# Kernel tuning notes

Hardware: AMD Instinct MI355X
Metric: run time of the kernel (lower is better)

The kernel has to match this reference:

```python
import jax, jax.numpy as jnp
import numpy as np

N, E, B, D, V = 200000, 3200000, 512, 32, 101
STEPS_MP, STEPS_S2S = 6, 6


def setup_inputs() -> dict:
    key = jax.random.key(0)
    ks = jax.random.split(key, 24)
    p = lambda k, s: jax.random.normal(k, s, jnp.float32) * 0.1
    inp = {}
    inp["node_type"] = jax.random.randint(ks[0], (N,), 0, V)
    inp["src"] = jax.random.randint(ks[1], (E,), 0, N)
    inp["dst"] = jax.random.randint(ks[2], (E,), 0, N)
    inp["graph_ids"] = jnp.sort(jax.random.randint(ks[3], (N,), 0, B))
    inp["emb"] = p(ks[4], (V, D)).at[0].set(0.0)  # padding_idx=0
    inp["W0"] = p(ks[5], (D, D)); inp["b0"] = p(ks[6], (D,))
    inp["Wm"] = p(ks[7], (D, D))
    inp["Wih_g"] = p(ks[8], (3 * D, D)); inp["Whh_g"] = p(ks[9], (3 * D, D))
    inp["bih_g"] = p(ks[10], (3 * D,)); inp["bhh_g"] = p(ks[11], (3 * D,))
    inp["Wih0"] = p(ks[12], (4 * D, 2 * D)); inp["Whh0"] = p(ks[13], (4 * D, D))
    inp["bih0"] = p(ks[14], (4 * D,)); inp["bhh0"] = p(ks[15], (4 * D,))
    inp["Wih12"] = p(ks[16], (2, 4 * D, D)); inp["Whh12"] = p(ks[17], (2, 4 * D, D))
    inp["bih12"] = p(ks[18], (2, 4 * D)); inp["bhh12"] = p(ks[19], (2, 4 * D))
    inp["Wr1"] = p(ks[20], (D, 2 * D)); inp["br1"] = p(ks[21], (D,))
    inp["Wr2"] = p(ks[22], (D, D)); inp["br2"] = p(ks[23], (D,))
    return inp


def _gru(x, h, Wih, Whh, bih, bhh):
    gi = x @ Wih.T + bih
    gh = h @ Whh.T + bhh
    r = jax.nn.sigmoid(gi[:, :D] + gh[:, :D])
    z = jax.nn.sigmoid(gi[:, D:2 * D] + gh[:, D:2 * D])
    n = jnp.tanh(gi[:, 2 * D:] + r * gh[:, 2 * D:])
    return (1.0 - z) * n + z * h


def _lstm(x, h, c, Wih, Whh, bih, bhh):
    g = x @ Wih.T + bih + h @ Whh.T + bhh
    i, f, gg, o = jnp.split(g, 4, axis=-1)  # torch gate order i,f,g,o
    c2 = jax.nn.sigmoid(f) * c + jax.nn.sigmoid(i) * jnp.tanh(gg)
    return jax.nn.sigmoid(o) * jnp.tanh(c2), c2


def _seg_softmax(e, ids, nseg):
    m = jax.ops.segment_max(e, ids, num_segments=nseg)
    ex = jnp.exp(e - m[ids])
    s = jax.ops.segment_sum(ex, ids, num_segments=nseg)
    return ex / s[ids]


def _forward(node_type, src, dst, graph_ids, emb, W0, b0, Wm,
             Wih_g, Whh_g, bih_g, bhh_g,
             Wih0, Whh0, bih0, bhh0, Wih12, Whh12, bih12, bhh12,
             Wr1, br1, Wr2, br2):
    # embedding lookup; dropout is identity at inference
    nfeat = emb[node_type]                         # [N, D]
    out = jax.nn.relu(nfeat @ W0.T + b0)           # lin0
    h = out                                        # GRU hidden init
    for _ in range(STEPS_MP):
        # NNConv-style sum aggregation over in-edges (e_feat is None -> edge-independent Wm)
        agg = jax.ops.segment_sum(out[src], dst, num_segments=N)   # [N, D]
        m = jax.nn.relu(agg @ Wm.T)
        h = _gru(m, h, Wih_g, Whh_g, bih_g, bhh_g)
        out = h
    # ---- Set2Set pooling (3-layer LSTM, 6 steps) ----
    lp = [(Wih0, Whh0, bih0, bhh0),
          (Wih12[0], Whh12[0], bih12[0], bhh12[0]),
          (Wih12[1], Whh12[1], bih12[1], bhh12[1])]
    hs = [jnp.zeros((B, D), out.dtype) for _ in range(3)]
    cs = [jnp.zeros((B, D), out.dtype) for _ in range(3)]
    q_star = jnp.zeros((B, 2 * D), out.dtype)
    for _ in range(STEPS_S2S):
        x = q_star
        for l, (Wih, Whh, bih, bhh) in enumerate(lp):
            hs[l], cs[l] = _lstm(x, hs[l], cs[l], Wih, Whh, bih, bhh)
            x = hs[l]
        q = x                                        # [B, D]
        e = jnp.sum(out * q[graph_ids], axis=-1)     # [N] attention logits
        alpha = _seg_softmax(e, graph_ids, B)
        r = jax.ops.segment_sum(alpha[:, None] * out, graph_ids, num_segments=B)
        q_star = jnp.concatenate([q, r], axis=-1)    # [B, 2D]
    # readout MLP (norm=False)
    return jax.nn.relu(q_star @ Wr1.T + br1) @ Wr2.T + br2


def reference(node_type, src, dst, graph_ids, emb, W0, b0, Wm,
              Wih_g, Whh_g, bih_g, bhh_g,
              Wih0, Whh0, bih0, bhh0, Wih12, Whh12, bih12, bhh12,
              Wr1, br1, Wr2, br2):
    return _forward(node_type, src, dst, graph_ids, emb, W0, b0, Wm,
                    Wih_g, Whh_g, bih_g, bhh_g,
                    Wih0, Whh0, bih0, bhh0, Wih12, Whh12, bih12, bhh12,
                    Wr1, br1, Wr2, br2)
```

## Files before the change

kernel.cpp:

```cpp
#include <hip/hip_runtime.h>
#include <hip/hip_bf16.h>
#include <hip/hip_fp16.h>

#define DD 32
constexpr int N_ = 200000;
constexpr int E_ = 3200000;
constexpr int B_ = 512;
constexpr int IDXCAP = 768;

typedef _Float16 f16x4 __attribute__((ext_vector_type(4)));
typedef float f32x4 __attribute__((ext_vector_type(4)));

constexpr int OFF_EMB=0, OFF_B0=3232, OFF_BIHG=3264, OFF_BHHG=3360, OFF_BIH0=3456,
  OFF_BHH0=3584, OFF_BIH12=3712, OFF_BHH12=3968, OFF_BR1=4224, OFF_BR2=4256,
  OFF_W0T=4288, OFF_WMT=5312, OFF_WIHGT=6336, OFF_WHHGT=9408,
  OFF_WIH0T=12480, OFF_WHH0T=20672, OFF_WIH1T=24768, OFF_WHH1T=28864,
  OFF_WIH2T=32960, OFF_WHH2T=37056, OFF_WR1T=41152, OFF_WR2T=43200;
constexpr long FLOAT_END=44288L;
constexpr size_t F16_BYTE = (size_t)FLOAT_END*4;
constexpr size_t H0_BYTE  = F16_BYTE + 12288;
constexpr size_t H1_BYTE  = H0_BYTE + (size_t)N_*DD*2;
constexpr size_t INT_BASE = H1_BYTE + (size_t)N_*DD*2;
constexpr int I_DEG=0, I_NOFF=200512, I_CURSOR=400512, I_GOFF=600512,
  I_BSUM=601088, I_BOFF=601344, I_CSR=601600;
constexpr int I_FLAG=3801600;

__device__ __forceinline__ float bf2f(unsigned short u){ return __uint_as_float(((unsigned)u)<<16); }
__device__ __forceinline__ float sigm(float x){ return 1.0f/(1.0f+__expf(-x)); }
__device__ __forceinline__ float tanhfast(float x){ return 1.0f - 2.0f/(__expf(2.0f*x)+1.0f); }

__device__ __forceinline__ void gbatch(const int* __restrict__ ip, int i, int rem,
                                       const __half* __restrict__ rowbase, int q,
                                       float& a0, float& a1, float& a2, float& a3){
  #pragma unroll
  for(int s=0;s<8;s++){
    int e  = 4*s + q;
    int ec = e < rem ? e : rem-1;
    int idx = ip[i + ec];
    uint2 v = *(const uint2*)(rowbase + (size_t)idx*DD);
    if(e >= rem){ v.x = 0u; v.y = 0u; }
    float2 f0 = __half22float2(*(__half2*)&v.x);
    float2 f1 = __half22float2(*(__half2*)&v.y);
    a0 += f0.x; a1 += f0.y; a2 += f1.x; a3 += f1.y;
  }
}

__global__ void k_detect(const unsigned int* __restrict__ emb_raw, int* __restrict__ flag){
  if(threadIdx.x==0){
    unsigned v=0;
    for(int i=16;i<32;i++) v |= emb_raw[i];
    flag[0] = v ? 1 : 0;
  }
}

struct PrepArgs { const void* s[22]; int off[22]; int sz[22]; int trR[22]; int soff[22]; int pk[22]; };

__global__ void k_prep(PrepArgs a, float* __restrict__ W, const int* __restrict__ flag){
  int bf = flag[0];
  int seg = blockIdx.y;
  int i = blockIdx.x*256 + threadIdx.x;
  if(i >= a.sz[seg]) return;
  int R = a.trR[seg];
  int P = a.pk[seg];
  int sidx;
  if(P){
    int c = i/(4*P); int rem = i%(4*P); int col = rem>>2; int s = rem&3;
    sidx = col*DD + 4*c + s;
  } else if(R){ int C = a.sz[seg]/R; sidx = (i%R)*C + (i/R); } else sidx = i;
  sidx += a.soff[seg];
  float v = bf ? bf2f(((const unsigned short*)a.s[seg])[sidx])
               : ((const float*)a.s[seg])[sidx];
  W[a.off[seg]+i] = v;
}

__global__ void k_prep16(const float* __restrict__ Wall, __half* __restrict__ F){
  int id = blockIdx.x*256 + threadIdx.x;
  if(id >= 6144) return;
  int e  = id & 3;
  int l  = (id >> 2) & 63;
  int kh = (id >> 8) & 1;
  int tmp = id >> 9;
  int jt  = tmp % 6;
  int reg = tmp / 6;
  int j = 16*jt + (l & 15);
  int k = 16*kh + 4*(l >> 4) + e;
  int srcoff = (reg==0 ? OFF_WIHGT : OFF_WHHGT) + j*DD + k;
  F[id] = __float2half(Wall[srcoff]);
}

__global__ void k_lin0(const int* __restrict__ nt, const float* __restrict__ Wall,
                       __half* __restrict__ hmir){
  int n = blockIdx.x*blockDim.x + threadIdx.x;
  if(n >= N_) return;
  const float* er  = Wall + OFF_EMB + nt[n]*DD;
  const float* W0T = Wall + OFF_W0T;
  const float* b0  = Wall + OFF_B0;
  float m[DD];
  #pragma unroll
  for(int j=0;j<DD;j++) m[j]=b0[j];
  #pragma unroll 4
  for(int k=0;k<DD;k++){
    float xk = er[k];
    #pragma unroll
    for(int j=0;j<DD;j++) m[j] = __fmaf_rn(W0T[k*DD+j], xk, m[j]);
  }
  __half* hrow = hmir + (size_t)n*DD;
  #pragma unroll
  for(int j=0;j<DD;j++) hrow[j]=__float2half(fmaxf(m[j],0.f));
}

__global__ void k_deg(const int* __restrict__ dst, int* __restrict__ deg,
                      int* __restrict__ key){
  int e = blockIdx.x*blockDim.x + threadIdx.x;
  if(e < E_){
    int d = dst[e];
    int old = atomicAdd(&deg[d], 1);
    key[e] = d | (old << 18);
  }
}
__global__ void __launch_bounds__(1024) k_scanA(const int* __restrict__ deg,
                       int* __restrict__ incl, int* __restrict__ bsum){
  __shared__ int sh[1024];
  int g = blockIdx.x*1024 + threadIdx.x;
  int v = (g < N_) ? deg[g] : 0;
  sh[threadIdx.x]=v; __syncthreads();
  for(int o=1;o<1024;o<<=1){
    int a = (threadIdx.x>=o) ? sh[threadIdx.x-o] : 0;
    __syncthreads();
    sh[threadIdx.x]+=a;
    __syncthreads();
  }
  if(g < N_) incl[g]=sh[threadIdx.x];
  if(threadIdx.x==1023) bsum[blockIdx.x]=sh[1023];
}
__global__ void k_scanB(const int* __restrict__ bsum, int* __restrict__ boff){
  __shared__ int sh[256];
  int t=threadIdx.x;
  int v=(t<196)?bsum[t]:0;
  sh[t]=v; __syncthreads();
  for(int o=1;o<256;o<<=1){
    int a=(t>=o)?sh[t-o]:0; __syncthreads(); sh[t]+=a; __syncthreads();
  }
  if(t<196) boff[t]=sh[t]-v;
}
__global__ void __launch_bounds__(1024) k_scanC(const int* __restrict__ deg,
                       const int* __restrict__ boff, int* __restrict__ noff,
                       int* __restrict__ incl_cursor){
  int g = blockIdx.x*1024 + threadIdx.x;
  if(g >= N_) return;
  int ex = incl_cursor[g] - deg[g] + boff[g>>10];
  noff[g]=ex; incl_cursor[g]=ex;
}
__global__ void k_goff(const int* __restrict__ gid, int* __restrict__ goff){
  int g = blockIdx.x*256 + threadIdx.x;
  if(g > B_) return;
  int lo=0, hi=N_;
  while(lo<hi){ int mid=(lo+hi)>>1; if(gid[mid]<g) lo=mid+1; else hi=mid; }
  goff[g]=lo;
}
__global__ void k_scatter(const int* __restrict__ src, const int* __restrict__ key,
                          const int* __restrict__ noff, int* __restrict__ csr){
  int e = blockIdx.x*256 + threadIdx.x;
  int k = key[e];
  int d = k & 0x3FFFF;
  int p = noff[d] + (k >> 18);
  csr[p] = src[e];
}

__global__ void __launch_bounds__(256) k_step(const float* __restrict__ Wall,
                       const __half* __restrict__ F16, const int* __restrict__ noff,
                       const int* __restrict__ deg, const int* __restrict__ csr,
                       const __half* __restrict__ curh, __half* __restrict__ nxth){
  __shared__ __align__(16) float  lds_acc[4][4][DD];
  __shared__ __align__(16) __half lds_m[4][16][40];
  __shared__ int lds_idx[4][IDXCAP];
  __shared__ int lds_nd[4][32];
  const int t = threadIdx.x;
  const int w = t >> 6, l = t & 63;
  const int d = l & 31, half = l >> 5;
  const int q  = d >> 3;
  const int r8 = d & 7;
  const int n0 = blockIdx.x*64 + w*16;
  const float4* WmP = (const float4*)(Wall + OFF_WMT);
  const __half* rowbase = curh + 4*r8;
  if(l < 16){
    lds_nd[w][l]    = noff[n0+l];
    lds_nd[w][16+l] = deg[n0+l];
  }
  int s_begin = lds_nd[w][0];
  int total   = lds_nd[w][15] + lds_nd[w][31] - s_begin;
  int tc = total < IDXCAP ? total : IDXCAP;
  for(int i=l; i<tc; i+=64) lds_idx[w][i] = csr[s_begin+i];
  if(total <= IDXCAP){
    for(int pp=0;pp<4;pp++){
      int iA = 4*pp + half, iB = iA + 2;
      int sA = lds_nd[w][iA] - s_begin, lA = lds_nd[w][16+iA];
      int sB = lds_nd[w][iB] - s_begin, lB = lds_nd[w][16+iB];
      const int* ipA = &lds_idx[w][sA];
      const int* ipB = &lds_idx[w][sB];
      float aA0=0.f,aA1=0.f,aA2=0.f,aA3=0.f;
      float aB0=0.f,aB1=0.f,aB2=0.f,aB3=0.f;
      int ml = lA > lB ? lA : lB;
      for(int i=0; i<ml; i+=32){
        int rA = lA - i, rB = lB - i;
        if(rA > 0) gbatch(ipA, i, rA, rowbase, q, aA0,aA1,aA2,aA3);
        if(rB > 0) gbatch(ipB, i, rB, rowbase, q, aB0,aB1,aB2,aB3);
      }
      #pragma unroll
      for(int off=8; off<=16; off<<=1){
        aA0 += __shfl_xor(aA0, off, 32); aA1 += __shfl_xor(aA1, off, 32);
        aA2 += __shfl_xor(aA2, off, 32); aA3 += __shfl_xor(aA3, off, 32);
        aB0 += __shfl_xor(aB0, off, 32); aB1 += __shfl_xor(aB1, off, 32);
        aB2 += __shfl_xor(aB2, off, 32); aB3 += __shfl_xor(aB3, off, 32);
      }
      int lsrc = d >> 2;
      float vA0=__shfl(aA0,lsrc,32), vA1=__shfl(aA1,lsrc,32);
      float vA2=__shfl(aA2,lsrc,32), vA3=__shfl(aA3,lsrc,32);
      float vB0=__shfl(aB0,lsrc,32), vB1=__shfl(aB1,lsrc,32);
      float vB2=__shfl(aB2,lsrc,32), vB3=__shfl(aB3,lsrc,32);
      float accA = (d&1) ? ((d&2)? vA3 : vA1) : ((d&2)? vA2 : vA0);
      float accB = (d&1) ? ((d&2)? vB3 : vB1) : ((d&2)? vB2 : vB0);
      lds_acc[w][half][d]   = accA;
      lds_acc[w][2+half][d] = accB;
      const float4* acA = (const float4*)(&lds_acc[w][half][0]);
      const float4* acB = (const float4*)(&lds_acc[w][2+half][0]);
      float mA = 0.f, mB = 0.f;
      #pragma unroll
      for(int c=0;c<8;c++){
        float4 wv = WmP[c*32 + d];
        float4 avA = acA[c];
        float4 avB = acB[c];
        mA = __fmaf_rn(wv.x, avA.x, mA); mB = __fmaf_rn(wv.x, avB.x, mB);
        mA = __fmaf_rn(wv.y, avA.y, mA); mB = __fmaf_rn(wv.y, avB.y, mB);
        mA = __fmaf_rn(wv.z, avA.z, mA); mB = __fmaf_rn(wv.z, avB.z, mB);
        mA = __fmaf_rn(wv.w, avA.w, mA); mB = __fmaf_rn(wv.w, avB.w, mB);
      }
      lds_m[w][iA][d] = __float2half(fmaxf(mA, 0.f));
      lds_m[w][iB][d] = __float2half(fmaxf(mB, 0.f));
    }
  } else {
    for(int p=0;p<8;p++){
      int ni = 2*p + half;
      int s0 = lds_nd[w][ni];
      int len = lds_nd[w][16+ni];
      float a0=0.f, a1=0.f, a2=0.f, a3=0.f;
      for(int i=0; i<len; i+=32){
        int rem = len - i;
        gbatch(csr + s0, i, rem, rowbase, q, a0,a1,a2,a3);
      }
      #pragma unroll
      for(int off=8; off<=16; off<<=1){
        a0 += __shfl_xor(a0, off, 32);
        a1 += __shfl_xor(a1, off, 32);
        a2 += __shfl_xor(a2, off, 32);
        a3 += __shfl_xor(a3, off, 32);
      }
      float v0 = __shfl(a0, d>>2, 32);
      float v1 = __shfl(a1, d>>2, 32);
      float v2 = __shfl(a2, d>>2, 32);
      float v3 = __shfl(a3, d>>2, 32);
      float accd = (d&1) ? ((d&2)? v3 : v1) : ((d&2)? v2 : v0);
      lds_acc[w][half][d] = accd;
      const float4* ac = (const float4*)(&lds_acc[w][half][0]);
      float m = 0.f;
      #pragma unroll
      for(int c=0;c<8;c++){
        float4 wv = WmP[c*32 + d];
        float4 av = ac[c];
        m = __fmaf_rn(wv.x, av.x, m);
        m = __fmaf_rn(wv.y, av.y, m);
        m = __fmaf_rn(wv.z, av.z, m);
        m = __fmaf_rn(wv.w, av.w, m);
      }
      lds_m[w][2*p+half][d] = __float2half(fmaxf(m, 0.f));
    }
  }
  const int rowa = l & 15, grp = l >> 4;
  f16x4 Am0 = *(const f16x4*)((const void*)&lds_m[w][rowa][4*grp]);
  f16x4 Am1 = *(const f16x4*)((const void*)&lds_m[w][rowa][16 + 4*grp]);
  const __half* hrow = curh + (size_t)(n0 + rowa)*DD;
  f16x4 Ah0 = *(const f16x4*)((const void*)(hrow + 4*grp));
  f16x4 Ah1 = *(const f16x4*)((const void*)(hrow + 16 + 4*grp));
  const f16x4* Bf = (const f16x4*)F16;
  f32x4 Drz[4], Din[2], Dhn[2];
  #pragma unroll
  for(int jt=0;jt<4;jt++){
    f32x4 a = {0.f,0.f,0.f,0.f};
    a = __builtin_amdgcn_mfma_f32_16x16x16f16(Ah0, Bf[(12 + jt*2    )*64 + l], a, 0,0,0);
    a = __builtin_amdgcn_mfma_f32_16x16x16f16(Ah1, Bf[(12 + jt*2 + 1)*64 + l], a, 0,0,0);
    a = __builtin_amdgcn_mfma_f32_16x16x16f16(Am0, Bf[(     jt*2    )*64 + l], a, 0,0,0);
    a = __builtin_amdgcn_mfma_f32_16x16x16f16(Am1, Bf[(     jt*2 + 1)*64 + l], a, 0,0,0);
    Drz[jt] = a;
  }
  #pragma unroll
  for(int s=0;s<2;s++){
    int jt = 4 + s;
    f32x4 a = {0.f,0.f,0.f,0.f};
    f32x4 b = {0.f,0.f,0.f,0.f};
    a = __builtin_amdgcn_mfma_f32_16x16x16f16(Am0, Bf[(     jt*2    )*64 + l], a, 0,0,0);
    a = __builtin_amdgcn_mfma_f32_16x16x16f16(Am1, Bf[(     jt*2 + 1)*64 + l], a, 0,0,0);
    b = __builtin_amdgcn_mfma_f32_16x16x16f16(Ah0, Bf[(12 + jt*2    )*64 + l], b, 0,0,0);
    b = __builtin_amdgcn_mfma_f32_16x16x16f16(Ah1, Bf[(12 + jt*2 + 1)*64 + l], b, 0,0,0);
    Din[s] = a; Dhn[s] = b;
  }
  #pragma unroll
  for(int s=0;s<2;s++){
    int dd = 16*s + rowa;
    float br = Wall[OFF_BIHG+dd]      + Wall[OFF_BHHG+dd];
    float bz = Wall[OFF_BIHG+DD+dd]   + Wall[OFF_BHHG+DD+dd];
    float bi = Wall[OFF_BIHG+2*DD+dd];
    float bh = Wall[OFF_BHHG+2*DD+dd];
    #pragma unroll
    for(int r=0;r<4;r++){
      int node = n0 + grp*4 + r;
      float hv = __half2float(curh[(size_t)node*DD + dd]);
      float rr = sigm(Drz[s][r]   + br);
      float zz = sigm(Drz[2+s][r] + bz);
      float nn = tanhfast((Din[s][r] + bi) + rr*(Dhn[s][r] + bh));
      nxth[(size_t)node*DD + dd] = __float2half((1.f - zz)*nn + zz*hv);
    }
  }
}

#define MAXEV 1024
__global__ void __launch_bounds__(1024, 8) k_s2s(const float* __restrict__ Wall,
                       const __half* __restrict__ hstate, const int* __restrict__ goff,
                       void* __restrict__ op, const int* __restrict__ flag){
  int g = blockIdx.x, t = threadIdx.x;
  int l32 = t & 31, g32 = t >> 5;
  __shared__ float evb[MAXEV];
  __shared__ float red[32*33];
  __shared__ float wred[16];
  __shared__ float qs[64];
  __shared__ float xb[64];
  __shared__ float hb[3][32];
  __shared__ float gbuf[128];
  __shared__ float yb[32];
  __shared__ float bc_mx, bc_inv;
  int s0 = goff[g], s1 = goff[g+1];
  int len = s1 - s0;
  int lc = len < MAXEV ? len : MAXEV;
  if(t < 64) qs[t] = 0.f;
  if(t < 96) hb[t>>5][t&31] = 0.f;
  float c0=0.f, c1=0.f, c2v=0.f;
  __syncthreads();
  for(int it=0; it<6; it++){
    if(t<64) xb[t]=qs[t];
    __syncthreads();
    if(t<128){
      const float* WT = Wall + OFF_WIH0T; const float* UT = Wall + OFF_WHH0T;
      float gv = Wall[OFF_BIH0+t] + Wall[OFF_BHH0+t];
      #pragma unroll 8
      for(int k=0;k<64;k++) gv = __fmaf_rn(WT[k*128+t], xb[k], gv);
      #pragma unroll 8
      for(int k=0;k<32;k++) gv = __fmaf_rn(UT[k*128+t], hb[0][k], gv);
      gbuf[t]=gv;
    }
    __syncthreads();
    if(t<32){
      float iv=sigm(gbuf[t]), fv=sigm(gbuf[32+t]), gg=tanhfast(gbuf[64+t]), ov=sigm(gbuf[96+t]);
      float c = fv*c0 + iv*gg; c0=c;
      float h2 = ov*tanhfast(c);
      hb[0][t]=h2; xb[t]=h2;
    }
    __syncthreads();
    for(int l=1;l<3;l++){
      if(t<128){
        const float* WT = Wall + (l==1?OFF_WIH1T:OFF_WIH2T);
        const float* UT = Wall + (l==1?OFF_WHH1T:OFF_WHH2T);
        int bo=(l-1)*128;
        float gv = Wall[OFF_BIH12+bo+t] + Wall[OFF_BHH12+bo+t];
        #pragma unroll 8
        for(int k=0;k<32;k++) gv = __fmaf_rn(WT[k*128+t], xb[k], gv);
        #pragma unroll 8
        for(int k=0;k<32;k++) gv = __fmaf_rn(UT[k*128+t], hb[l][k], gv);
        gbuf[t]=gv;
      }
      __syncthreads();
      if(t<32){
        float cp = (l==1)?c1:c2v;
        float iv=sigm(gbuf[t]), fv=sigm(gbuf[32+t]), gg=tanhfast(gbuf[64+t]), ov=sigm(gbuf[96+t]);
        float c = fv*cp + iv*gg;
        if(l==1) c1=c; else c2v=c;
        float h2 = ov*tanhfast(c);
        hb[l][t]=h2; xb[t]=h2;
      }
      __syncthreads();
    }
    float q = xb[l32];
    float lmax = -INFINITY;
    for(int i=g32; i<len; i+=32){
      float v = __half2float(hstate[(size_t)(s0+i)*DD+l32])*q;
      #pragma unroll
      for(int o=16;o>0;o>>=1) v += __shfl_xor(v,o,32);
      if(i<lc && l32==0) evb[i]=v;
      lmax = fmaxf(lmax, v);
    }
    lmax = fmaxf(lmax, __shfl_xor(lmax, 32, 64));
    if((t&63)==0) wred[t>>6]=lmax;
    __syncthreads();
    if(t==0){ float m=wred[0];
      #pragma unroll
      for(int k=1;k<16;k++) m=fmaxf(m,wred[k]);
      bc_mx=m; }
    __syncthreads();
    float mx = bc_mx;
    float sm=0.f;
    for(int i=t;i<len;i+=1024){
      float v;
      if(i<lc) v=evb[i];
      else { v=0.f; for(int k=0;k<DD;k++) v += __half2float(hstate[(size_t)(s0+i)*DD+k])*xb[k]; }
      float e = __expf(v-mx);
      if(i<lc) evb[i]=e;
      sm += e;
    }
    #pragma unroll
    for(int o=32;o>0;o>>=1) sm += __shfl_xor(sm,o,64);
    if((t&63)==0) wred[t>>6]=sm;
    __syncthreads();
    if(t==0){ float s=0.f;
      #pragma unroll
      for(int k=0;k<16;k++) s+=wred[k];
      bc_inv = (s>0.f) ? 1.f/s : 0.f; }
    __syncthreads();
    float inv = bc_inv;
    float acc=0.f;
    for(int i=g32;i<len;i+=32){
      float fv = __half2float(hstate[(size_t)(s0+i)*DD+l32]);
      float wgt;
      if(i<lc) wgt=evb[i];
      else { float vv=fv*q;
             #pragma unroll
             for(int o=16;o>0;o>>=1) vv += __shfl_xor(vv,o,32);
             wgt=__expf(vv-mx); }
      acc = __fmaf_rn(wgt, fv, acc);
    }
    red[g32*33+l32]=acc; __syncthreads();
    if(t<32){
      float s=0.f;
      #pragma unroll
      for(int k=0;k<32;k++) s+=red[k*33+t];
      qs[32+t]=s*inv; qs[t]=xb[t];
    }
    __syncthreads();
  }
  if(t<32){
    const float* W1 = Wall+OFF_WR1T;
    float s = Wall[OFF_BR1+t];
    #pragma unroll 8
    for(int k=0;k<64;k++) s = __fmaf_rn(W1[k*32+t], qs[k], s);
    yb[t]=fmaxf(s,0.f);
  }
  __syncthreads();
  if(t<32){
    const float* W2 = Wall+OFF_WR2T;
    float o = Wall[OFF_BR2+t];
    #pragma unroll 8
    for(int k=0;k<32;k++) o = __fmaf_rn(W2[k*32+t], yb[k], o);
    if(flag[0]) ((__hip_bfloat16*)op)[g*32+t]=__float2bfloat16(o);
    else        ((float*)op)[g*32+t]=o;
  }
}

extern "C" void kernel_launch(void* const* d_in, const int* in_sizes, int n_in,
                              void* d_out, int out_size, void* d_ws, size_t ws_size,
                              hipStream_t stream) {
  const int* nt  = (const int*)d_in[0];
  const int* src = (const int*)d_in[1];
  const int* dst = (const int*)d_in[2];
  const int* gid = (const int*)d_in[3];
  float* W = (float*)d_ws;
  char* base = (char*)d_ws;
  __half* F16 = (__half*)(base + F16_BYTE);
  __half* h0 = (__half*)(base + H0_BYTE);
  __half* h1 = (__half*)(base + H1_BYTE);
  int* I = (int*)(base + INT_BASE);
  int* deg=I+I_DEG; int* noff=I+I_NOFF; int* cursor=I+I_CURSOR;
  int* goff=I+I_GOFF; int* bsum=I+I_BSUM; int* boff=I+I_BOFF; int* csr=I+I_CSR;
  int* flag=I+I_FLAG;
  int* key = (int*)h1;

  hipMemsetAsync(deg, 0, (size_t)N_*4, stream);

  k_detect<<<1,64,0,stream>>>((const unsigned int*)d_in[4], flag);

  PrepArgs pa;
  const int sidx[22]={4,6,10,11,14,15,18,19,21,23, 5,7,8,9,12,13,16,16,17,17,20,22};
  const int offs[22]={OFF_EMB,OFF_B0,OFF_BIHG,OFF_BHHG,OFF_BIH0,OFF_BHH0,OFF_BIH12,
                      OFF_BHH12,OFF_BR1,OFF_BR2, OFF_W0T,OFF_WMT,OFF_WIHGT,OFF_WHHGT,
                      OFF_WIH0T,OFF_WHH0T,OFF_WIH1T,OFF_WIH2T,OFF_WHH1T,OFF_WHH2T,
                      OFF_WR1T,OFF_WR2T};
  const int szs[22]={3232,32,96,96,128,128,256,256,32,32, 1024,1024,3072,3072,
                     8192,4096,4096,4096,4096,4096,2048,1024};
  const int trR[22]={0,0,0,0,0,0,0,0,0,0, 32,0,0,0,128,128,128,128,128,128,32,32};
  const int pkv[22]={0,0,0,0,0,0,0,0,0,0, 0,32,0,0,0,0,0,0,0,0,0,0};
  const int sof[22]={0,0,0,0,0,0,0,0,0,0, 0,0,0,0,0,0,0,4096,0,4096,0,0};
  for(int i=0;i<22;i++){ pa.s[i]=d_in[sidx[i]]; pa.off[i]=offs[i]; pa.sz[i]=szs[i];
                         pa.trR[i]=trR[i]; pa.soff[i]=sof[i]; pa.pk[i]=pkv[i]; }
  hipLaunchKernelGGL(k_prep, dim3(32,22), dim3(256), 0, stream, pa, W, flag);
  k_prep16<<<24,256,0,stream>>>(W, F16);

  k_lin0<<<782,256,0,stream>>>(nt, W, h0);
  k_deg<<<12500,256,0,stream>>>(dst, deg, key);
  k_scanA<<<196,1024,0,stream>>>(deg, cursor, bsum);
  k_scanB<<<1,256,0,stream>>>(bsum, boff);
  k_scanC<<<196,1024,0,stream>>>(deg, boff, noff, cursor);
  k_goff<<<3,256,0,stream>>>(gid, goff);
  k_scatter<<<12500,256,0,stream>>>(src, key, noff, csr);

  __half* curh = h0; __half* nxth = h1;
  for(int s=0;s<6;s++){
    k_step<<<3125,256,0,stream>>>(W, F16, noff, deg, csr, curh, nxth);
    __half* tmp = curh; curh = nxth; nxth = tmp;
  }
  k_s2s<<<B_,1024,0,stream>>>(W, curh, goff, d_out, flag);
}
```

Measured before the change: 800.3 us.

## Build CSR with two-pass LDS bucket sort instead of global atomics

Replaces CSR construction, which used per-edge global atomics on node degree followed by a three-kernel scan and a scatter, with a two-level counting sort. Edges are first bucketed by dst>>8 using per-block LDS histograms, a column-wise scan and a bucketed scatter. Each 256-node bucket is then finely sorted in LDS to produce deg, noff and csr. This targets global atomic contention and random global writes, at the cost of an extra pass over the edges and non-deterministic order within a node.

Result: faster. 690.0 us (-13.8%).

```diff
diff --git a/kernel.cpp b/kernel.cpp
--- a/kernel.cpp
+++ b/kernel.cpp
@@ -7,6 +7,9 @@
 constexpr int E_ = 3200000;
 constexpr int B_ = 512;
 constexpr int IDXCAP = 768;
+constexpr int NBUCK = 782;
+constexpr int NBLKA = 256;
+constexpr int EPB   = E_/NBLKA;
 
 typedef _Float16 f16x4 __attribute__((ext_vector_type(4)));
 typedef float f32x4 __attribute__((ext_vector_type(4)));
@@ -21,9 +24,10 @@
 constexpr size_t H0_BYTE  = F16_BYTE + 12288;
 constexpr size_t H1_BYTE  = H0_BYTE + (size_t)N_*DD*2;
 constexpr size_t INT_BASE = H1_BYTE + (size_t)N_*DD*2;
-constexpr int I_DEG=0, I_NOFF=200512, I_CURSOR=400512, I_GOFF=600512,
-  I_BSUM=601088, I_BOFF=601344, I_CSR=601600;
+constexpr int I_DEG=0, I_NOFF=200512, I_CNT=400512, I_GOFF=600512,
+  I_CSR=601600;
 constexpr int I_FLAG=3801600;
+constexpr int I_TOT=3801664, I_BBASE=3802496;
 
 __device__ __forceinline__ float bf2f(unsigned short u){ return __uint_as_float(((unsigned)u)<<16); }
 __device__ __forceinline__ float sigm(float x){ return 1.0f/(1.0f+__expf(-x)); }
@@ -109,47 +113,78 @@
   for(int j=0;j<DD;j++) hrow[j]=__float2half(fmaxf(m[j],0.f));
 }
 
-__global__ void k_deg(const int* __restrict__ dst, int* __restrict__ deg,
-                      int* __restrict__ key){
-  int e = blockIdx.x*blockDim.x + threadIdx.x;
-  if(e < E_){
+__global__ void __launch_bounds__(256) k_bcnt(const int* __restrict__ dst,
+                                              int* __restrict__ cnt){
+  __shared__ int h[NBUCK];
+  int blk = blockIdx.x, t = threadIdx.x;
+  for(int i=t;i<NBUCK;i+=256) h[i]=0;
+  __syncthreads();
+  int e0 = blk*EPB;
+  for(int i=t;i<EPB;i+=256) atomicAdd(&h[dst[e0+i]>>8], 1);
+  __syncthreads();
+  for(int i=t;i<NBUCK;i+=256) cnt[blk*NBUCK+i]=h[i];
+}
+__global__ void __launch_bounds__(256) k_bscan1(int* __restrict__ cnt,
+                                                int* __restrict__ total){
+  __shared__ int sh[256];
+  int b = blockIdx.x, t = threadIdx.x;
+  int v = cnt[t*NBUCK + b];
+  sh[t]=v; __syncthreads();
+  for(int o=1;o<256;o<<=1){ int a=(t>=o)?sh[t-o]:0; __syncthreads(); sh[t]+=a; __syncthreads(); }
+  cnt[t*NBUCK+b] = sh[t]-v;
+  if(t==255) total[b]=sh[255];
+}
+__global__ void __launch_bounds__(1024) k_bscan2(const int* __restrict__ total,
+                                                 int* __restrict__ bbase){
+  __shared__ int sh[1024];
+  int t=threadIdx.x;
+  int v = (t<NBUCK)? total[t] : 0;
+  sh[t]=v; __syncthreads();
+  for(int o=1;o<1024;o<<=1){ int a=(t>=o)?sh[t-o]:0; __syncthreads(); sh[t]+=a; __syncthreads(); }
+  if(t<NBUCK) bbase[t]=sh[t]-v;
+  if(t==NBUCK-1) bbase[NBUCK]=sh[t];
+}
+__global__ void __launch_bounds__(256) k_bscat(const int* __restrict__ src,
+                        const int* __restrict__ dst, const int* __restrict__ cnt,
+                        const int* __restrict__ bbase, int* __restrict__ bucketed){
+  __shared__ int loff[NBUCK];
+  int blk = blockIdx.x, t = threadIdx.x;
+  for(int i=t;i<NBUCK;i+=256) loff[i] = bbase[i] + cnt[blk*NBUCK+i];
+  __syncthreads();
+  int e0 = blk*EPB;
+  for(int i=t;i<EPB;i+=256){
+    int e = e0+i;
     int d = dst[e];
-    int old = atomicAdd(&deg[d], 1);
-    key[e] = d | (old << 18);
-  }
-}
-__global__ void __launch_bounds__(1024) k_scanA(const int* __restrict__ deg,
-                       int* __restrict__ incl, int* __restrict__ bsum){
-  __shared__ int sh[1024];
-  int g = blockIdx.x*1024 + threadIdx.x;
-  int v = (g < N_) ? deg[g] : 0;
-  sh[threadIdx.x]=v; __syncthreads();
-  for(int o=1;o<1024;o<<=1){
-    int a = (threadIdx.x>=o) ? sh[threadIdx.x-o] : 0;
-    __syncthreads();
-    sh[threadIdx.x]+=a;
-    __syncthreads();
-  }
-  if(g < N_) incl[g]=sh[threadIdx.x];
-  if(threadIdx.x==1023) bsum[blockIdx.x]=sh[1023];
-}
-__global__ void k_scanB(const int* __restrict__ bsum, int* __restrict__ boff){
-  __shared__ int sh[256];
-  int t=threadIdx.x;
-  int v=(t<196)?bsum[t]:0;
-  sh[t]=v; __syncthreads();
-  for(int o=1;o<256;o<<=1){
-    int a=(t>=o)?sh[t-o]:0; __syncthreads(); sh[t]+=a; __syncthreads();
-  }
-  if(t<196) boff[t]=sh[t]-v;
-}
-__global__ void __launch_bounds__(1024) k_scanC(const int* __restrict__ deg,
-                       const int* __restrict__ boff, int* __restrict__ noff,
-                       int* __restrict__ incl_cursor){
-  int g = blockIdx.x*1024 + threadIdx.x;
-  if(g >= N_) return;
-  int ex = incl_cursor[g] - deg[g] + boff[g>>10];
-  noff[g]=ex; incl_cursor[g]=ex;
+    int p = atomicAdd(&loff[d>>8], 1);
+    bucketed[p] = src[e] | ((d & 255) << 18);
+  }
+}
+__global__ void __launch_bounds__(256) k_bfine(const int* __restrict__ bucketed,
+                        const int* __restrict__ bbase, int* __restrict__ deg,
+                        int* __restrict__ noff, int* __restrict__ csr){
+  __shared__ int cnt[256];
+  __shared__ int sc[256];
+  int b = blockIdx.x, t = threadIdx.x;
+  int base = bbase[b], end = bbase[b+1];
+  cnt[t]=0;
+  __syncthreads();
+  for(int i=base+t; i<end; i+=256) atomicAdd(&cnt[(bucketed[i]>>18)&255], 1);
+  __syncthreads();
+  int v = cnt[t];
+  sc[t]=v; __syncthreads();
+  for(int o=1;o<256;o<<=1){ int a=(t>=o)?sc[t-o]:0; __syncthreads(); sc[t]+=a; __syncthreads(); }
+  int excl = sc[t]-v;
+  int n = b*256+t;
+  if(n < N_){ deg[n]=v; noff[n]=base+excl; }
+  __syncthreads();
+  sc[t]=excl; cnt[t]=0;
+  __syncthreads();
+  for(int i=base+t; i<end; i+=256){
+    int pv = bucketed[i];
+    int loc = (pv>>18)&255;
+    int r = atomicAdd(&cnt[loc], 1);
+    csr[base + sc[loc] + r] = pv & 0x3FFFF;
+  }
 }
 __global__ void k_goff(const int* __restrict__ gid, int* __restrict__ goff){
   int g = blockIdx.x*256 + threadIdx.x;
@@ -157,14 +192,6 @@
   int lo=0, hi=N_;
   while(lo<hi){ int mid=(lo+hi)>>1; if(gid[mid]<g) lo=mid+1; else hi=mid; }
   goff[g]=lo;
-}
-__global__ void k_scatter(const int* __restrict__ src, const int* __restrict__ key,
-                          const int* __restrict__ noff, int* __restrict__ csr){
-  int e = blockIdx.x*256 + threadIdx.x;
-  int k = key[e];
-  int d = k & 0x3FFFF;
-  int p = noff[d] + (k >> 18);
-  csr[p] = src[e];
 }
 
 __global__ void __launch_bounds__(256) k_step(const float* __restrict__ Wall,
@@ -475,12 +502,10 @@
   __half* h0 = (__half*)(base + H0_BYTE);
   __half* h1 = (__half*)(base + H1_BYTE);
   int* I = (int*)(base + INT_BASE);
-  int* deg=I+I_DEG; int* noff=I+I_NOFF; int* cursor=I+I_CURSOR;
-  int* goff=I+I_GOFF; int* bsum=I+I_BSUM; int* boff=I+I_BOFF; int* csr=I+I_CSR;
-  int* flag=I+I_FLAG;
-  int* key = (int*)h1;
-
-  hipMemsetAsync(deg, 0, (size_t)N_*4, stream);
+  int* deg=I+I_DEG; int* noff=I+I_NOFF; int* cnt=I+I_CNT;
+  int* goff=I+I_GOFF; int* csr=I+I_CSR;
+  int* flag=I+I_FLAG; int* total=I+I_TOT; int* bbase=I+I_BBASE;
+  int* bucketed = (int*)h1;
 
   k_detect<<<1,64,0,stream>>>((const unsigned int*)d_in[4], flag);
 
@@ -501,12 +526,12 @@
   k_prep16<<<24,256,0,stream>>>(W, F16);
 
   k_lin0<<<782,256,0,stream>>>(nt, W, h0);
-  k_deg<<<12500,256,0,stream>>>(dst, deg, key);
-  k_scanA<<<196,1024,0,stream>>>(deg, cursor, bsum);
-  k_scanB<<<1,256,0,stream>>>(bsum, boff);
-  k_scanC<<<196,1024,0,stream>>>(deg, boff, noff, cursor);
+  k_bcnt<<<NBLKA,256,0,stream>>>(dst, cnt);
+  k_bscan1<<<NBUCK,256,0,stream>>>(cnt, total);
+  k_bscan2<<<1,1024,0,stream>>>(total, bbase);
+  k_bscat<<<NBLKA,256,0,stream>>>(src, dst, cnt, bbase, bucketed);
   k_goff<<<3,256,0,stream>>>(gid, goff);
-  k_scatter<<<12500,256,0,stream>>>(src, key, noff, csr);
+  k_bfine<<<NBUCK,256,0,stream>>>(bucketed, bbase, deg, noff, csr);
 
   __half* curh = h0; __half* nxth = h1;
   for(int s=0;s<6;s++){
```
